# Kernel tuning notes

Measured on AMD Instinct MI355X. Metric: run time of the kernel, lower is better.

Reference implementation:

```python
import jax, jax.numpy as jnp
import numpy as np

N, E, D, H, C, G, L = 50000, 1250000, 128, 64, 10, 128, 2


def setup_inputs() -> dict:
    key = jax.random.key(0)
    ks = jax.random.split(key, 18)
    s = lambda fan_in: 1.0 / np.sqrt(fan_in)
    inp = {
        "x": jax.random.normal(ks[0], (N, D), dtype=jnp.float32),
        "edge_index": jax.random.randint(ks[1], (2, E), 0, N, dtype=jnp.int64),
        "batch": jnp.sort(jax.random.randint(ks[2], (N,), 0, G, dtype=jnp.int64)),
        # node embedding MLP (D->H->H)
        "emb_w1": jax.random.uniform(ks[3], (D, H), jnp.float32, -s(D), s(D)),
        "emb_b1": jnp.zeros((H,), jnp.float32),
        "emb_w2": jax.random.uniform(ks[4], (H, H), jnp.float32, -s(H), s(H)),
        "emb_b2": jnp.zeros((H,), jnp.float32),
        # per-conv-block params, stacked over L layers
        "rel_w": jax.random.uniform(ks[5], (L, H, H), jnp.float32, -s(H), s(H)),
        "rel_b": jnp.zeros((L, H), jnp.float32),
        "root_w": jax.random.uniform(ks[6], (L, H, H), jnp.float32, -s(H), s(H)),
        "post_w1": jax.random.uniform(ks[7], (L, H, H), jnp.float32, -s(H), s(H)),
        "post_b1": jnp.zeros((L, H), jnp.float32),
        "post_w2": jax.random.uniform(ks[8], (L, H, H), jnp.float32, -s(H), s(H)),
        "post_b2": jnp.zeros((L, H), jnp.float32),
        # classifier
        "cls_w": jax.random.uniform(ks[9], (H, C), jnp.float32, -s(H), s(H)),
        "cls_b": jnp.zeros((C,), jnp.float32),
    }
    return inp


def _mlp(h, w1, b1, w2, b2):
    # Linear -> relu -> (dropout: identity in eval) -> Linear
    return jax.nn.relu(h @ w1 + b1) @ w2 + b2


def reference(x, edge_index, batch, emb_w1, emb_b1, emb_w2, emb_b2,
              rel_w, rel_b, root_w, post_w1, post_b1, post_w2, post_b2,
              cls_w, cls_b):
    src, dst = edge_index[0], edge_index[1]
    h = _mlp(x, emb_w1, emb_b1, emb_w2, emb_b2)  # [N,H]
    deg = jax.ops.segment_sum(jnp.ones((E,), h.dtype), dst, num_segments=N)
    inv_deg = 1.0 / jnp.maximum(deg, 1.0)  # mean aggregation, isolated nodes -> 0
    for l in range(L):
        agg = jax.ops.segment_sum(h[src], dst, num_segments=N) * inv_deg[:, None]
        h = agg @ rel_w[l] + rel_b[l] + h @ root_w[l]  # GraphConv (lin_root bias-free)
        h = _mlp(h, post_w1[l], post_b1[l], post_w2[l], post_b2[l])
        h = jax.nn.relu(h)  # dropout is identity in eval
    cnt = jax.ops.segment_sum(jnp.ones((N,), h.dtype), batch, num_segments=G)
    pooled = jax.ops.segment_sum(h, batch, num_segments=G) / jnp.maximum(cnt, 1.0)[:, None]
    return pooled @ cls_w + cls_b  # [G,C]
```

## Files before the change

kernel.cpp:

```cpp
#include <hip/hip_runtime.h>

typedef unsigned int u32;
typedef unsigned short u16;

#define NN 50000
#define EE 1250000
#define DD 128
#define HH 64
#define NCLS 10
#define NG 128
#define MAXDEG 80

#define NTILES ((NN + 63) / 64)
#define LDSW 68

#define PBUK 392
#define SBLK 128
#define CHUNK ((EE + SBLK - 1) / SBLK)
#define NDP  (PBUK * 128)

#define NWMAT 8
#define WT_LO (NWMAT * 4096)


__device__ __forceinline__ u32 f2bf(float f) {
    u32 u = __float_as_uint(f);
    return (u + 0x7FFFu + ((u >> 16) & 1u)) >> 16;
}
__device__ __forceinline__ float bf2f(u16 v) {
    return __uint_as_float(((u32)v) << 16);
}

typedef __attribute__((ext_vector_type(8))) short bf16x8;
typedef __attribute__((ext_vector_type(4))) float f32x4;


__device__ __forceinline__ void load_w(const float* __restrict__ g, float (*wS)[LDSW], int t) {
    #pragma unroll
    for (int r = 0; r < 4; ++r) {
        int idx = r * 256 + t;
        int k = idx >> 4, f4 = idx & 15;
        float4 v = *(const float4*)(g + k * 64 + f4 * 4);
        *(float4*)&wS[k][f4 * 4] = v;
    }
}

__device__ __forceinline__ void load_inT(const float* __restrict__ g, int ld, int c0,
                                         float (*iS)[LDSW], int t, int nb) {
    #pragma unroll
    for (int r = 0; r < 4; ++r) {
        int idx = r * 256 + t;
        int n = idx >> 4, k4 = idx & 15;
        int node = nb + n;
        if (node >= NN) node = NN - 1;
        float4 v = *(const float4*)(g + (size_t)node * ld + c0 + k4 * 4);
        int k0 = k4 * 4;
        int nx = n ^ k0;
        iS[k0 + 0][nx] = v.x;
        iS[k0 + 1][nx] = v.y;
        iS[k0 + 2][nx] = v.z;
        iS[k0 + 3][nx] = v.w;
    }
}

__device__ __forceinline__ void gemm_acc(const float (*iS)[LDSW], const float (*wS)[LDSW],
                                         float acc[4][4], int tx, int ty) {
    #pragma unroll 8
    for (int k = 0; k < 64; ++k) {
        const float4 wv = *(const float4*)&wS[k][tx * 4];
        const float4 iv = *(const float4*)&iS[k][(ty * 4) ^ (k & 60)];
        acc[0][0] += iv.x * wv.x; acc[0][1] += iv.x * wv.y; acc[0][2] += iv.x * wv.z; acc[0][3] += iv.x * wv.w;
        acc[1][0] += iv.y * wv.x; acc[1][1] += iv.y * wv.y; acc[1][2] += iv.y * wv.z; acc[1][3] += iv.y * wv.w;
        acc[2][0] += iv.z * wv.x; acc[2][1] += iv.z * wv.y; acc[2][2] += iv.z * wv.z; acc[2][3] += iv.z * wv.w;
        acc[3][0] += iv.w * wv.x; acc[3][1] += iv.w * wv.y; acc[3][2] += iv.w * wv.z; acc[3][3] += iv.w * wv.w;
    }
}

__device__ __forceinline__ void store_accT(float (*iS)[LDSW], const float acc[4][4], int tx, int ty) {
    #pragma unroll
    for (int i = 0; i < 4; ++i) {
        int k = tx * 4 + i;
        *(float4*)&iS[k][(ty * 4) ^ (tx * 4)] =
            make_float4(acc[0][i], acc[1][i], acc[2][i], acc[3][i]);
    }
}

__device__ __forceinline__ void init_bias(float acc[4][4], const float* __restrict__ b, int tx) {
    float4 bv = *(const float4*)(b + tx * 4);
    #pragma unroll
    for (int j = 0; j < 4; ++j) { acc[j][0] = bv.x; acc[j][1] = bv.y; acc[j][2] = bv.z; acc[j][3] = bv.w; }
}

__device__ __forceinline__ void relu_acc(float acc[4][4]) {
    #pragma unroll
    for (int j = 0; j < 4; ++j)
        #pragma unroll
        for (int i = 0; i < 4; ++i) acc[j][i] = fmaxf(acc[j][i], 0.0f);
}

__device__ __forceinline__ void store_hb(u16* __restrict__ hb, const float acc[4][4],
                                         int tx, int ty, int nb) {
    #pragma unroll
    for (int j = 0; j < 4; ++j) {
        int node = nb + ty * 4 + j;
        if (node < NN) {
            u32 p0 = f2bf(acc[j][0]) | (f2bf(acc[j][1]) << 16);
            u32 p1 = f2bf(acc[j][2]) | (f2bf(acc[j][3]) << 16);
            u32* q = (u32*)(hb + (size_t)node * HH) + tx * 2;
            q[0] = p0; q[1] = p1;
        }
    }
}


__global__ __launch_bounds__(256) void k_embed_psort(
    const float* __restrict__ x,
    const float* __restrict__ w1, const float* __restrict__ b1,
    const float* __restrict__ w2, const float* __restrict__ b2,
    u16* __restrict__ hb,
    const int* __restrict__ ei, u32* __restrict__ bedges,
    int* __restrict__ gboff, int* __restrict__ ghist,
    const float* __restrict__ rel_w, const float* __restrict__ root_w,
    const float* __restrict__ pw1, const float* __restrict__ pw2,
    u16* __restrict__ wtb) {
    __shared__ __align__(16) char smem[2 * 64 * LDSW * 4];
    const int t = threadIdx.x;

    if (blockIdx.x < NTILES) {
        float (*wS)[LDSW] = (float (*)[LDSW])smem;
        float (*iS)[LDSW] = (float (*)[LDSW])(smem + 64 * LDSW * 4);
        const int tx = t & 15, ty = t >> 4;
        const int nb = blockIdx.x * 64;

        float acc[4][4];
        init_bias(acc, b1, tx);
        load_w(w1, wS, t);
        load_inT(x, DD, 0, iS, t, nb);
        __syncthreads();
        gemm_acc(iS, wS, acc, tx, ty);
        __syncthreads();
        load_w(w1 + 64 * 64, wS, t);
        load_inT(x, DD, 64, iS, t, nb);
        __syncthreads();
        gemm_acc(iS, wS, acc, tx, ty);
        __syncthreads();
        relu_acc(acc);
        store_accT(iS, acc, tx, ty);
        load_w(w2, wS, t);
        __syncthreads();
        float acc2[4][4];
        init_bias(acc2, b2, tx);
        gemm_acc(iS, wS, acc2, tx, ty);
        store_hb(hb, acc2, tx, ty, nb);
    } else if (blockIdx.x < NTILES + SBLK) {
        int* hist  = (int*)smem;
        int* boffS = hist + PBUK;
        int* wsum  = boffS + PBUK;
        const int cb = blockIdx.x - NTILES;
        const int base = cb * CHUNK;
        const int n = min(CHUNK, EE - base);

        for (int b = t; b < PBUK; b += 256) hist[b] = 0;
        __syncthreads();
        for (int i = t; i < n; i += 256) {
            int src = ei[base + i];
            int dst = ei[EE + base + i];
            if ((unsigned)src < NN && (unsigned)dst < NN)
                atomicAdd(&hist[dst >> 7], 1);
        }
        __syncthreads();
        int v = 0, h0 = 0;
        if (t < PBUK / 2) { h0 = hist[2 * t]; v = h0 + hist[2 * t + 1]; }
        int lane = t & 63, wd = t >> 6;
        int incl = v;
        #pragma unroll
        for (int d = 1; d < 64; d <<= 1) {
            int tt = __shfl_up(incl, d);
            if (lane >= d) incl += tt;
        }
        if (lane == 63) wsum[wd] = incl;
        __syncthreads();
        int woff = 0;
        for (int w = 0; w < wd; ++w) woff += wsum[w];
        if (t < PBUK / 2) {
            int excl = woff + incl - v;
            boffS[2 * t] = excl;
            boffS[2 * t + 1] = excl + h0;
        }
        __syncthreads();
        for (int b = t; b < PBUK; b += 256) {
            gboff[cb * PBUK + b] = boffS[b];
            ghist[cb * PBUK + b] = hist[b];
        }
        __syncthreads();
        for (int b = t; b < PBUK; b += 256) hist[b] = 0;
        __syncthreads();
        for (int i = t; i < n; i += 256) {
            int src = ei[base + i];
            int dst = ei[EE + base + i];
            if ((unsigned)src < NN && (unsigned)dst < NN) {
                int b = dst >> 7;
                int p = atomicAdd(&hist[b], 1);
                bedges[base + boffS[b] + p] = ((u32)src << 7) | (u32)(dst & 127);
            }
        }
    } else {
        const int m = blockIdx.x - NTILES - SBLK;
        const int layer = m >> 2, which = m & 3;
        const float* srcw =
            (which == 0 ? rel_w : which == 1 ? root_w : which == 2 ? pw1 : pw2)
            + (size_t)layer * HH * HH;
        float* ldsf = (float*)smem;
        #pragma unroll
        for (int r = 0; r < 16; ++r) {
            int idx = r * 256 + t;
            int k = idx >> 6, n = idx & 63;
            ldsf[k * 65 + n] = srcw[k * 64 + n];
        }
        __syncthreads();
        #pragma unroll
        for (int r = 0; r < 16; ++r) {
            int idx = r * 256 + t;
            int n = idx >> 6, k = idx & 63;
            float v = ldsf[k * 65 + n];
            u16 hi = (u16)f2bf(v);
            u16 lo = (u16)f2bf(v - bf2f(hi));
            wtb[m * 4096 + n * 64 + k] = hi;
            wtb[WT_LO + m * 4096 + n * 64 + k] = lo;
        }
    }
}


__global__ __launch_bounds__(256) void k_adj(const u32* __restrict__ bedges,
                                             const int* __restrict__ gboff,
                                             const int* __restrict__ ghist,
                                             u16* __restrict__ slots,
                                             int* __restrict__ deg,
                                             float* __restrict__ pooled) {
    __shared__ u16 ls[128 * MAXDEG];
    __shared__ int lc[128];
    const int b = blockIdx.x, t = threadIdx.x;
    const int lane = t & 63, wid = t >> 6;
    if (b < (NG * HH) / 256) pooled[b * 256 + t] = 0.0f;
    if (t < 128) lc[t] = 0;
    __syncthreads();
    for (int sb = wid; sb < SBLK; sb += 4) {
        int off = gboff[sb * PBUK + b];
        int cnt = ghist[sb * PBUK + b];
        int gbase = sb * CHUNK + off;
        for (int i = lane; i < cnt; i += 64) {
            u32 p = bedges[gbase + i];
            int o = (int)(p & 127u);
            int src = (int)(p >> 7);
            int pos = atomicAdd(&lc[o], 1);
            if (pos < MAXDEG) ls[o * MAXDEG + pos] = (u16)src;
        }
    }
    __syncthreads();
    u32* gs = (u32*)(slots + (size_t)b * 128 * MAXDEG);
    const u32* lsu = (const u32*)ls;
    for (int i = t; i < 128 * MAXDEG / 2; i += 256) gs[i] = lsu[i];
    if (t < 128) deg[b * 128 + t] = lc[t];
}


__global__ __launch_bounds__(256) void k_agg(
    const u16* __restrict__ hb, const int* __restrict__ deg,
    const u16* __restrict__ slots, u16* __restrict__ aggb) {
    const int wid = threadIdx.x >> 6, lane = threadIdx.x & 63;
    const int nA = blockIdx.x * 8 + wid * 2;
    if (nA >= NN) return;
    const int nB = nA + 1;
    const int dA = deg[nA];
    const int dB = (nB < NN) ? deg[nB] : 0;
    const int mA = min(dA, MAXDEG), mB = min(dB, MAXDEG);
    const u16* srA = slots + (size_t)nA * MAXDEG;
    const u16* srB = slots + (size_t)nB * MAXDEG;
    const u32* rowA = (const u32*)srA;
    const u32* rowB = (const u32*)srB;
    float sA = 0.0f, sB = 0.0f;
    const int mm = max(mA, mB);
    for (int e = 0; e + 8 <= mm; e += 8) {
        const int hx = e >> 1;
        const bool pA = (e + 8 <= mA), pB = (e + 8 <= mB);
        float a0=0,a1=0,a2=0,a3=0,a4=0,a5=0,a6=0,a7=0;
        float b0=0,b1=0,b2=0,b3=0,b4=0,b5=0,b6=0,b7=0;
        if (pA) {
            u32 u0 = rowA[hx], u1 = rowA[hx+1], u2 = rowA[hx+2], u3 = rowA[hx+3];
            a0 = bf2f(hb[(size_t)(u0 & 0xffffu) * HH + lane]);
            a1 = bf2f(hb[(size_t)(u0 >> 16) * HH + lane]);
            a2 = bf2f(hb[(size_t)(u1 & 0xffffu) * HH + lane]);
            a3 = bf2f(hb[(size_t)(u1 >> 16) * HH + lane]);
            a4 = bf2f(hb[(size_t)(u2 & 0xffffu) * HH + lane]);
            a5 = bf2f(hb[(size_t)(u2 >> 16) * HH + lane]);
            a6 = bf2f(hb[(size_t)(u3 & 0xffffu) * HH + lane]);
            a7 = bf2f(hb[(size_t)(u3 >> 16) * HH + lane]);
        }
        if (pB) {
            u32 u0 = rowB[hx], u1 = rowB[hx+1], u2 = rowB[hx+2], u3 = rowB[hx+3];
            b0 = bf2f(hb[(size_t)(u0 & 0xffffu) * HH + lane]);
            b1 = bf2f(hb[(size_t)(u0 >> 16) * HH + lane]);
            b2 = bf2f(hb[(size_t)(u1 & 0xffffu) * HH + lane]);
            b3 = bf2f(hb[(size_t)(u1 >> 16) * HH + lane]);
            b4 = bf2f(hb[(size_t)(u2 & 0xffffu) * HH + lane]);
            b5 = bf2f(hb[(size_t)(u2 >> 16) * HH + lane]);
            b6 = bf2f(hb[(size_t)(u3 & 0xffffu) * HH + lane]);
            b7 = bf2f(hb[(size_t)(u3 >> 16) * HH + lane]);
        }
        if (pA) sA += ((a0 + a1) + (a2 + a3)) + ((a4 + a5) + (a6 + a7));
        if (pB) sB += ((b0 + b1) + (b2 + b3)) + ((b4 + b5) + (b6 + b7));
    }
    for (int e = mA & ~7; e < mA; ++e)
        sA += bf2f(hb[(size_t)srA[e] * HH + lane]);
    for (int e = mB & ~7; e < mB; ++e)
        sB += bf2f(hb[(size_t)srB[e] * HH + lane]);
    aggb[(size_t)nA * HH + lane] = (u16)f2bf(sA * (1.0f / (float)max(dA, 1)));
    if (nB < NN)
        aggb[(size_t)nB * HH + lane] = (u16)f2bf(sB * (1.0f / (float)max(dB, 1)));
}


__global__ __launch_bounds__(256) void k_dense(
    u16* __restrict__ hb, const u16* __restrict__ aggb,
    const u16* __restrict__ wt,
    const float* __restrict__ relb,
    const float* __restrict__ pb1, const float* __restrict__ pb2,
    const int* __restrict__ batch, float* __restrict__ pooled, int do_pool) {
    __shared__ __align__(16) u16 acts[2][64][72];
    const int t = threadIdx.x;
    const int w = t >> 6;
    const int l = t & 63;
    const int lr = l & 15, lg = l >> 4;
    const int rowb = w * 16;
    const int nb = blockIdx.x * 64;
    int nodeA = nb + rowb + lr;
    if (nodeA >= NN) nodeA = NN - 1;

    const u16* w_rel = wt;
    const u16* w_root = wt + 4096;
    const u16* w_p1  = wt + 2 * 4096;
    const u16* w_p2  = wt + 3 * 4096;

    const u16* agp = aggb + (size_t)nodeA * HH + lg * 8;
    const u16* hbp = hb   + (size_t)nodeA * HH + lg * 8;
    bf16x8 a0 = *(const bf16x8*)agp;
    bf16x8 a1 = *(const bf16x8*)(agp + 32);
    bf16x8 h0 = *(const bf16x8*)hbp;
    bf16x8 h1 = *(const bf16x8*)(hbp + 32);

    f32x4 acc[4];
    #pragma unroll
    for (int tt = 0; tt < 4; ++tt) {
        float b = relb[tt * 16 + lr];
        acc[tt] = (f32x4){b, b, b, b};
    }
    #pragma unroll
    for (int tt = 0; tt < 4; ++tt) {
        const u16* pr = w_rel  + (tt * 16 + lr) * 64 + lg * 8;
        const u16* po = w_root + (tt * 16 + lr) * 64 + lg * 8;
        acc[tt] = __builtin_amdgcn_mfma_f32_16x16x32_bf16(a0, *(const bf16x8*)pr,                acc[tt], 0, 0, 0);
        acc[tt] = __builtin_amdgcn_mfma_f32_16x16x32_bf16(a1, *(const bf16x8*)(pr + 32),         acc[tt], 0, 0, 0);
        acc[tt] = __builtin_amdgcn_mfma_f32_16x16x32_bf16(a0, *(const bf16x8*)(pr + WT_LO),      acc[tt], 0, 0, 0);
        acc[tt] = __builtin_amdgcn_mfma_f32_16x16x32_bf16(a1, *(const bf16x8*)(pr + WT_LO + 32), acc[tt], 0, 0, 0);
        acc[tt] = __builtin_amdgcn_mfma_f32_16x16x32_bf16(h0, *(const bf16x8*)po,                acc[tt], 0, 0, 0);
        acc[tt] = __builtin_amdgcn_mfma_f32_16x16x32_bf16(h1, *(const bf16x8*)(po + 32),         acc[tt], 0, 0, 0);
        acc[tt] = __builtin_amdgcn_mfma_f32_16x16x32_bf16(h0, *(const bf16x8*)(po + WT_LO),      acc[tt], 0, 0, 0);
        acc[tt] = __builtin_amdgcn_mfma_f32_16x16x32_bf16(h1, *(const bf16x8*)(po + WT_LO + 32), acc[tt], 0, 0, 0);
    }
    #pragma unroll
    for (int tt = 0; tt < 4; ++tt)
        #pragma unroll
        for (int r = 0; r < 4; ++r)
            acts[0][rowb + lg * 4 + r][tt * 16 + lr] = (u16)f2bf(acc[tt][r]);
    __syncthreads();

    bf16x8 c0 = *(const bf16x8*)&acts[0][rowb + lr][lg * 8];
    bf16x8 c1 = *(const bf16x8*)&acts[0][rowb + lr][32 + lg * 8];
    f32x4 acc2[4];
    #pragma unroll
    for (int tt = 0; tt < 4; ++tt) {
        float b = pb1[tt * 16 + lr];
        acc2[tt] = (f32x4){b, b, b, b};
    }
    #pragma unroll
    for (int tt = 0; tt < 4; ++tt) {
        const u16* pr = w_p1 + (tt * 16 + lr) * 64 + lg * 8;
        acc2[tt] = __builtin_amdgcn_mfma_f32_16x16x32_bf16(c0, *(const bf16x8*)pr,                acc2[tt], 0, 0, 0);
        acc2[tt] = __builtin_amdgcn_mfma_f32_16x16x32_bf16(c1, *(const bf16x8*)(pr + 32),         acc2[tt], 0, 0, 0);
        acc2[tt] = __builtin_amdgcn_mfma_f32_16x16x32_bf16(c0, *(const bf16x8*)(pr + WT_LO),      acc2[tt], 0, 0, 0);
        acc2[tt] = __builtin_amdgcn_mfma_f32_16x16x32_bf16(c1, *(const bf16x8*)(pr + WT_LO + 32), acc2[tt], 0, 0, 0);
    }
    #pragma unroll
    for (int tt = 0; tt < 4; ++tt)
        #pragma unroll
        for (int r = 0; r < 4; ++r)
            acts[1][rowb + lg * 4 + r][tt * 16 + lr] = (u16)f2bf(fmaxf(acc2[tt][r], 0.0f));
    __syncthreads();

    bf16x8 d0 = *(const bf16x8*)&acts[1][rowb + lr][lg * 8];
    bf16x8 d1 = *(const bf16x8*)&acts[1][rowb + lr][32 + lg * 8];
    f32x4 acc3[4];
    #pragma unroll
    for (int tt = 0; tt < 4; ++tt) {
        float b = pb2[tt * 16 + lr];
        acc3[tt] = (f32x4){b, b, b, b};
    }
    #pragma unroll
    for (int tt = 0; tt < 4; ++tt) {
        const u16* pr = w_p2 + (tt * 16 + lr) * 64 + lg * 8;
        acc3[tt] = __builtin_amdgcn_mfma_f32_16x16x32_bf16(d0, *(const bf16x8*)pr,                acc3[tt], 0, 0, 0);
        acc3[tt] = __builtin_amdgcn_mfma_f32_16x16x32_bf16(d1, *(const bf16x8*)(pr + 32),         acc3[tt], 0, 0, 0);
        acc3[tt] = __builtin_amdgcn_mfma_f32_16x16x32_bf16(d0, *(const bf16x8*)(pr + WT_LO),      acc3[tt], 0, 0, 0);
        acc3[tt] = __builtin_amdgcn_mfma_f32_16x16x32_bf16(d1, *(const bf16x8*)(pr + WT_LO + 32), acc3[tt], 0, 0, 0);
    }

    if (!do_pool) {
        #pragma unroll
        for (int tt = 0; tt < 4; ++tt)
            #pragma unroll
            for (int r = 0; r < 4; ++r) {
                int node = nb + rowb + lg * 4 + r;
                if (node < NN)
                    hb[(size_t)node * HH + tt * 16 + lr] = (u16)f2bf(fmaxf(acc3[tt][r], 0.0f));
            }
    } else {
        #pragma unroll
        for (int tt = 0; tt < 4; ++tt)
            #pragma unroll
            for (int r = 0; r < 4; ++r)
                acts[0][rowb + lg * 4 + r][tt * 16 + lr] = (u16)f2bf(fmaxf(acc3[tt][r], 0.0f));
        __syncthreads();
        if (t < HH) {
            const int f = t;
            const int n1 = min(64, NN - nb);
            int cur = batch[nb];
            float s = 0.0f;
            for (int i = 0; i < n1; ++i) {
                int g = batch[nb + i];
                if (g != cur) {
                    if ((unsigned)cur < NG) atomicAdd(&pooled[cur * HH + f], s);
                    s = 0.0f; cur = g;
                }
                s += bf2f(acts[0][i][f]);
            }
            if ((unsigned)cur < NG) atomicAdd(&pooled[cur * HH + f], s);
        }
    }
}


__global__ void k_cls(const float* __restrict__ pooled, const int* __restrict__ batch,
                      const float* __restrict__ w, const float* __restrict__ b,
                      float* __restrict__ out) {
    const int g = blockIdx.x;
    const int t = threadIdx.x;
    if (t >= NCLS) return;
    int lo = 0, hi = NN;
    while (lo < hi) { int mid = (lo + hi) >> 1; if (batch[mid] < g) lo = mid + 1; else hi = mid; }
    const int beg = lo;
    lo = 0; hi = NN;
    while (lo < hi) { int mid = (lo + hi) >> 1; if (batch[mid] < g + 1) lo = mid + 1; else hi = mid; }
    const int cnt = lo - beg;
    const float inv = 1.0f / (float)max(cnt, 1);
    float o = b[t];
    #pragma unroll 8
    for (int k = 0; k < HH; ++k) o += pooled[g * HH + k] * inv * w[k * NCLS + t];
    out[g * NCLS + t] = o;
}


extern "C" void kernel_launch(void* const* d_in, const int* in_sizes, int n_in,
                              void* d_out, int out_size, void* d_ws, size_t ws_size,
                              hipStream_t stream) {
    const float* x      = (const float*)d_in[0];
    const int*   ei     = (const int*)d_in[1];
    const int*   batch  = (const int*)d_in[2];
    const float* emb_w1 = (const float*)d_in[3];
    const float* emb_b1 = (const float*)d_in[4];
    const float* emb_w2 = (const float*)d_in[5];
    const float* emb_b2 = (const float*)d_in[6];
    const float* rel_w  = (const float*)d_in[7];
    const float* rel_b  = (const float*)d_in[8];
    const float* root_w = (const float*)d_in[9];
    const float* pw1    = (const float*)d_in[10];
    const float* pb1    = (const float*)d_in[11];
    const float* pw2    = (const float*)d_in[12];
    const float* pb2    = (const float*)d_in[13];
    const float* cls_w  = (const float*)d_in[14];
    const float* cls_b  = (const float*)d_in[15];
    float* out = (float*)d_out;

    char* ws = (char*)d_ws;
    size_t off = 0;
    auto alloc = [&](size_t bytes) -> void* {
        off = (off + 255) & ~(size_t)255;
        void* p = ws + off;
        off += bytes;
        return p;
    };
    u16*   hb     = (u16*)alloc((size_t)NN * HH * 2);
    u16*   aggb   = (u16*)alloc((size_t)NN * HH * 2);
    u32*   bedges = (u32*)aggb;
    u16*   slots  = (u16*)alloc((size_t)NDP * MAXDEG * 2);
    int*   deg    = (int*)alloc((size_t)NDP * 4);
    int*   gboff  = (int*)alloc((size_t)SBLK * PBUK * 4);
    int*   ghist  = (int*)alloc((size_t)SBLK * PBUK * 4);
    float* pooled = (float*)alloc((size_t)NG * HH * 4);
    u16*   wtb    = (u16*)alloc((size_t)2 * NWMAT * 4096 * 2);

    k_embed_psort<<<NTILES + SBLK + NWMAT, 256, 0, stream>>>(
        x, emb_w1, emb_b1, emb_w2, emb_b2, hb, ei, bedges, gboff, ghist,
        rel_w, root_w, pw1, pw2, wtb);
    k_adj<<<PBUK, 256, 0, stream>>>(bedges, gboff, ghist, slots, deg, pooled);
    k_agg<<<(NN + 7) / 8, 256, 0, stream>>>(hb, deg, slots, aggb);
    k_dense<<<NTILES, 256, 0, stream>>>(hb, aggb, wtb, rel_b, pb1, pb2, batch, pooled, 0);
    k_agg<<<(NN + 7) / 8, 256, 0, stream>>>(hb, deg, slots, aggb);
    k_dense<<<NTILES, 256, 0, stream>>>(hb, aggb, wtb + 4 * 4096,
                                        rel_b + HH, pb1 + HH, pb2 + HH,
                                        batch, pooled, 1);
    k_cls<<<NG, 64, 0, stream>>>(pooled, batch, cls_w, cls_b, out);
}
```

Before: 316.0 us.

## Move embedding MLP to split-bf16 MFMA and vectorize aggregation with sentinel padding

The embedding MLP moves from a scalar fp32 LDS GEMM to MFMA bf16 instructions, using hi/lo split precision on both inputs and weights to approximate fp32 accuracy. Weight transposition and splitting moves into a separate small prep kernel that runs first. The aggregation kernel is rewritten so each half-wave handles one node and loads two features per lane with 16-wide unrolled gathers. Slot rows are padded with a sentinel index that points to an extra zero row appended to hb, which removes the tail loops. This adds one kernel launch and padded gathers that read the zero row.

```diff
diff --git a/kernel.cpp b/kernel.cpp
--- a/kernel.cpp
+++ b/kernel.cpp
@@ -12,15 +12,18 @@
 #define MAXDEG 80
 
 #define NTILES ((NN + 63) / 64)
-#define LDSW 68
 
 #define PBUK 392
 #define SBLK 128
 #define CHUNK ((EE + SBLK - 1) / SBLK)
 #define NDP  (PBUK * 128)
 
-#define NWMAT 8
-#define WT_LO (NWMAT * 4096)
+#define WT_LO  (8 * 4096)
+#define WT_E1  (16 * 4096)
+#define WT_E1L (WT_E1 + 8192)
+#define WT_E2  (WT_E1 + 16384)
+#define WT_E2L (WT_E2 + 4096)
+#define WT_TOT (WT_E2 + 8192)
 
 
 __device__ __forceinline__ u32 f2bf(float f) {
@@ -35,79 +38,71 @@
 typedef __attribute__((ext_vector_type(4))) float f32x4;
 
 
-__device__ __forceinline__ void load_w(const float* __restrict__ g, float (*wS)[LDSW], int t) {
-    #pragma unroll
-    for (int r = 0; r < 4; ++r) {
-        int idx = r * 256 + t;
-        int k = idx >> 4, f4 = idx & 15;
-        float4 v = *(const float4*)(g + k * 64 + f4 * 4);
-        *(float4*)&wS[k][f4 * 4] = v;
-    }
-}
-
-__device__ __forceinline__ void load_inT(const float* __restrict__ g, int ld, int c0,
-                                         float (*iS)[LDSW], int t, int nb) {
-    #pragma unroll
-    for (int r = 0; r < 4; ++r) {
-        int idx = r * 256 + t;
-        int n = idx >> 4, k4 = idx & 15;
-        int node = nb + n;
-        if (node >= NN) node = NN - 1;
-        float4 v = *(const float4*)(g + (size_t)node * ld + c0 + k4 * 4);
-        int k0 = k4 * 4;
-        int nx = n ^ k0;
-        iS[k0 + 0][nx] = v.x;
-        iS[k0 + 1][nx] = v.y;
-        iS[k0 + 2][nx] = v.z;
-        iS[k0 + 3][nx] = v.w;
-    }
-}
-
-__device__ __forceinline__ void gemm_acc(const float (*iS)[LDSW], const float (*wS)[LDSW],
-                                         float acc[4][4], int tx, int ty) {
-    #pragma unroll 8
-    for (int k = 0; k < 64; ++k) {
-        const float4 wv = *(const float4*)&wS[k][tx * 4];
-        const float4 iv = *(const float4*)&iS[k][(ty * 4) ^ (k & 60)];
-        acc[0][0] += iv.x * wv.x; acc[0][1] += iv.x * wv.y; acc[0][2] += iv.x * wv.z; acc[0][3] += iv.x * wv.w;
-        acc[1][0] += iv.y * wv.x; acc[1][1] += iv.y * wv.y; acc[1][2] += iv.y * wv.z; acc[1][3] += iv.y * wv.w;
-        acc[2][0] += iv.z * wv.x; acc[2][1] += iv.z * wv.y; acc[2][2] += iv.z * wv.z; acc[2][3] += iv.z * wv.w;
-        acc[3][0] += iv.w * wv.x; acc[3][1] += iv.w * wv.y; acc[3][2] += iv.w * wv.z; acc[3][3] += iv.w * wv.w;
-    }
-}
-
-__device__ __forceinline__ void store_accT(float (*iS)[LDSW], const float acc[4][4], int tx, int ty) {
-    #pragma unroll
-    for (int i = 0; i < 4; ++i) {
-        int k = tx * 4 + i;
-        *(float4*)&iS[k][(ty * 4) ^ (tx * 4)] =
-            make_float4(acc[0][i], acc[1][i], acc[2][i], acc[3][i]);
-    }
-}
-
-__device__ __forceinline__ void init_bias(float acc[4][4], const float* __restrict__ b, int tx) {
-    float4 bv = *(const float4*)(b + tx * 4);
-    #pragma unroll
-    for (int j = 0; j < 4; ++j) { acc[j][0] = bv.x; acc[j][1] = bv.y; acc[j][2] = bv.z; acc[j][3] = bv.w; }
-}
-
-__device__ __forceinline__ void relu_acc(float acc[4][4]) {
-    #pragma unroll
-    for (int j = 0; j < 4; ++j)
-        #pragma unroll
-        for (int i = 0; i < 4; ++i) acc[j][i] = fmaxf(acc[j][i], 0.0f);
-}
-
-__device__ __forceinline__ void store_hb(u16* __restrict__ hb, const float acc[4][4],
-                                         int tx, int ty, int nb) {
-    #pragma unroll
-    for (int j = 0; j < 4; ++j) {
-        int node = nb + ty * 4 + j;
-        if (node < NN) {
-            u32 p0 = f2bf(acc[j][0]) | (f2bf(acc[j][1]) << 16);
-            u32 p1 = f2bf(acc[j][2]) | (f2bf(acc[j][3]) << 16);
-            u32* q = (u32*)(hb + (size_t)node * HH) + tx * 2;
-            q[0] = p0; q[1] = p1;
+__global__ __launch_bounds__(256) void k_wprep(
+    const float* __restrict__ rel_w, const float* __restrict__ root_w,
+    const float* __restrict__ pw1, const float* __restrict__ pw2,
+    const float* __restrict__ ew1, const float* __restrict__ ew2,
+    u16* __restrict__ wtb) {
+    __shared__ float ldsf[128 * 65];
+    const int t = threadIdx.x;
+    const int m = blockIdx.x;
+    if (m < 8) {
+        const int layer = m >> 2, which = m & 3;
+        const float* srcw =
+            (which == 0 ? rel_w : which == 1 ? root_w : which == 2 ? pw1 : pw2)
+            + (size_t)layer * HH * HH;
+        #pragma unroll
+        for (int r = 0; r < 16; ++r) {
+            int idx = r * 256 + t;
+            int k = idx >> 6, n = idx & 63;
+            ldsf[k * 65 + n] = srcw[idx];
+        }
+        __syncthreads();
+        #pragma unroll
+        for (int r = 0; r < 16; ++r) {
+            int idx = r * 256 + t;
+            int n = idx >> 6, k = idx & 63;
+            float v = ldsf[k * 65 + n];
+            u16 hi = (u16)f2bf(v);
+            u16 lo = (u16)f2bf(v - bf2f(hi));
+            wtb[m * 4096 + idx] = hi;
+            wtb[WT_LO + m * 4096 + idx] = lo;
+        }
+    } else if (m == 8) {
+        #pragma unroll
+        for (int r = 0; r < 32; ++r) {
+            int idx = r * 256 + t;
+            int k = idx >> 6, n = idx & 63;
+            ldsf[k * 65 + n] = ew1[idx];
+        }
+        __syncthreads();
+        #pragma unroll
+        for (int r = 0; r < 32; ++r) {
+            int idx = r * 256 + t;
+            int n = idx >> 7, k = idx & 127;
+            float v = ldsf[k * 65 + n];
+            u16 hi = (u16)f2bf(v);
+            u16 lo = (u16)f2bf(v - bf2f(hi));
+            wtb[WT_E1 + idx] = hi;
+            wtb[WT_E1L + idx] = lo;
+        }
+    } else {
+        #pragma unroll
+        for (int r = 0; r < 16; ++r) {
+            int idx = r * 256 + t;
+            int k = idx >> 6, n = idx & 63;
+            ldsf[k * 65 + n] = ew2[idx];
+        }
+        __syncthreads();
+        #pragma unroll
+        for (int r = 0; r < 16; ++r) {
+            int idx = r * 256 + t;
+            int n = idx >> 6, k = idx & 63;
+            float v = ldsf[k * 65 + n];
+            u16 hi = (u16)f2bf(v);
+            u16 lo = (u16)f2bf(v - bf2f(hi));
+            wtb[WT_E2 + idx] = hi;
+            wtb[WT_E2L + idx] = lo;
         }
     }
 }
@@ -115,44 +110,100 @@
 
 __global__ __launch_bounds__(256) void k_embed_psort(
     const float* __restrict__ x,
-    const float* __restrict__ w1, const float* __restrict__ b1,
-    const float* __restrict__ w2, const float* __restrict__ b2,
+    const float* __restrict__ b1, const float* __restrict__ b2,
+    const u16* __restrict__ wtb,
     u16* __restrict__ hb,
     const int* __restrict__ ei, u32* __restrict__ bedges,
-    int* __restrict__ gboff, int* __restrict__ ghist,
-    const float* __restrict__ rel_w, const float* __restrict__ root_w,
-    const float* __restrict__ pw1, const float* __restrict__ pw2,
-    u16* __restrict__ wtb) {
-    __shared__ __align__(16) char smem[2 * 64 * LDSW * 4];
+    int* __restrict__ gboff, int* __restrict__ ghist) {
+    __shared__ __align__(16) char smem[2 * 64 * 72 * 2];
     const int t = threadIdx.x;
 
     if (blockIdx.x < NTILES) {
-        float (*wS)[LDSW] = (float (*)[LDSW])smem;
-        float (*iS)[LDSW] = (float (*)[LDSW])(smem + 64 * LDSW * 4);
-        const int tx = t & 15, ty = t >> 4;
+        u16* acts0 = (u16*)smem;
+        u16* acts1 = (u16*)smem + 64 * 72;
+        const int l = t & 63;
+        const int lr = l & 15, lg = l >> 4;
+        const int rowb = (t >> 6) * 16;
         const int nb = blockIdx.x * 64;
-
-        float acc[4][4];
-        init_bias(acc, b1, tx);
-        load_w(w1, wS, t);
-        load_inT(x, DD, 0, iS, t, nb);
-        __syncthreads();
-        gemm_acc(iS, wS, acc, tx, ty);
-        __syncthreads();
-        load_w(w1 + 64 * 64, wS, t);
-        load_inT(x, DD, 64, iS, t, nb);
-        __syncthreads();
-        gemm_acc(iS, wS, acc, tx, ty);
-        __syncthreads();
-        relu_acc(acc);
-        store_accT(iS, acc, tx, ty);
-        load_w(w2, wS, t);
-        __syncthreads();
-        float acc2[4][4];
-        init_bias(acc2, b2, tx);
-        gemm_acc(iS, wS, acc2, tx, ty);
-        store_hb(hb, acc2, tx, ty, nb);
-    } else if (blockIdx.x < NTILES + SBLK) {
+        int nodeA = nb + rowb + lr;
+        if (nodeA >= NN) nodeA = NN - 1;
+        const float* xp = x + (size_t)nodeA * DD + lg * 8;
+
+        f32x4 acc[4];
+        #pragma unroll
+        for (int tt = 0; tt < 4; ++tt) {
+            float b = b1[tt * 16 + lr];
+            acc[tt] = (f32x4){b, b, b, b};
+        }
+        #pragma unroll
+        for (int kc = 0; kc < 4; ++kc) {
+            float4 v0 = *(const float4*)(xp + kc * 32);
+            float4 v1 = *(const float4*)(xp + kc * 32 + 4);
+            float vv[8] = {v0.x, v0.y, v0.z, v0.w, v1.x, v1.y, v1.z, v1.w};
+            bf16x8 xh, xl;
+            #pragma unroll
+            for (int j = 0; j < 8; ++j) {
+                u16 hi = (u16)f2bf(vv[j]);
+                xh[j] = (short)hi;
+                xl[j] = (short)(u16)f2bf(vv[j] - bf2f(hi));
+            }
+            #pragma unroll
+            for (int tt = 0; tt < 4; ++tt) {
+                const u16* ph = wtb + WT_E1 + (tt * 16 + lr) * 128 + kc * 32 + lg * 8;
+                const u16* pl = wtb + WT_E1L + (tt * 16 + lr) * 128 + kc * 32 + lg * 8;
+                bf16x8 wh = *(const bf16x8*)ph;
+                bf16x8 wl = *(const bf16x8*)pl;
+                acc[tt] = __builtin_amdgcn_mfma_f32_16x16x32_bf16(xh, wh, acc[tt], 0, 0, 0);
+                acc[tt] = __builtin_amdgcn_mfma_f32_16x16x32_bf16(xl, wh, acc[tt], 0, 0, 0);
+                acc[tt] = __builtin_amdgcn_mfma_f32_16x16x32_bf16(xh, wl, acc[tt], 0, 0, 0);
+            }
+        }
+        #pragma unroll
+        for (int tt = 0; tt < 4; ++tt)
+            #pragma unroll
+            for (int r = 0; r < 4; ++r) {
+                float v = fmaxf(acc[tt][r], 0.0f);
+                u16 hi = (u16)f2bf(v);
+                u16 lo = (u16)f2bf(v - bf2f(hi));
+                acts0[(rowb + lg * 4 + r) * 72 + tt * 16 + lr] = hi;
+                acts1[(rowb + lg * 4 + r) * 72 + tt * 16 + lr] = lo;
+            }
+        __syncthreads();
+
+        bf16x8 c0h = *(const bf16x8*)&acts0[(rowb + lr) * 72 + lg * 8];
+        bf16x8 c1h = *(const bf16x8*)&acts0[(rowb + lr) * 72 + 32 + lg * 8];
+        bf16x8 c0l = *(const bf16x8*)&acts1[(rowb + lr) * 72 + lg * 8];
+        bf16x8 c1l = *(const bf16x8*)&acts1[(rowb + lr) * 72 + 32 + lg * 8];
+        f32x4 acc2[4];
+        #pragma unroll
+        for (int tt = 0; tt < 4; ++tt) {
+            float b = b2[tt * 16 + lr];
+            acc2[tt] = (f32x4){b, b, b, b};
+        }
+        #pragma unroll
+        for (int tt = 0; tt < 4; ++tt) {
+            const u16* ph = wtb + WT_E2 + (tt * 16 + lr) * 64 + lg * 8;
+            const u16* pl = wtb + WT_E2L + (tt * 16 + lr) * 64 + lg * 8;
+            bf16x8 wh0 = *(const bf16x8*)ph;
+            bf16x8 wh1 = *(const bf16x8*)(ph + 32);
+            bf16x8 wl0 = *(const bf16x8*)pl;
+            bf16x8 wl1 = *(const bf16x8*)(pl + 32);
+            acc2[tt] = __builtin_amdgcn_mfma_f32_16x16x32_bf16(c0h, wh0, acc2[tt], 0, 0, 0);
+            acc2[tt] = __builtin_amdgcn_mfma_f32_16x16x32_bf16(c1h, wh1, acc2[tt], 0, 0, 0);
+            acc2[tt] = __builtin_amdgcn_mfma_f32_16x16x32_bf16(c0l, wh0, acc2[tt], 0, 0, 0);
+            acc2[tt] = __builtin_amdgcn_mfma_f32_16x16x32_bf16(c1l, wh1, acc2[tt], 0, 0, 0);
+            acc2[tt] = __builtin_amdgcn_mfma_f32_16x16x32_bf16(c0h, wl0, acc2[tt], 0, 0, 0);
+            acc2[tt] = __builtin_amdgcn_mfma_f32_16x16x32_bf16(c1h, wl1, acc2[tt], 0, 0, 0);
+        }
+        #pragma unroll
+        for (int tt = 0; tt < 4; ++tt)
+            #pragma unroll
+            for (int r = 0; r < 4; ++r) {
+                int node = nb + rowb + lg * 4 + r;
+                if (node < NN)
+                    hb[(size_t)node * HH + tt * 16 + lr] = (u16)f2bf(acc2[tt][r]);
+            }
+    } else {
         int* hist  = (int*)smem;
         int* boffS = hist + PBUK;
         int* wsum  = boffS + PBUK;
@@ -204,30 +255,6 @@
                 bedges[base + boffS[b] + p] = ((u32)src << 7) | (u32)(dst & 127);
             }
         }
-    } else {
-        const int m = blockIdx.x - NTILES - SBLK;
-        const int layer = m >> 2, which = m & 3;
-        const float* srcw =
-            (which == 0 ? rel_w : which == 1 ? root_w : which == 2 ? pw1 : pw2)
-            + (size_t)layer * HH * HH;
-        float* ldsf = (float*)smem;
-        #pragma unroll
-        for (int r = 0; r < 16; ++r) {
-            int idx = r * 256 + t;
-            int k = idx >> 6, n = idx & 63;
-            ldsf[k * 65 + n] = srcw[k * 64 + n];
-        }
-        __syncthreads();
-        #pragma unroll
-        for (int r = 0; r < 16; ++r) {
-            int idx = r * 256 + t;
-            int n = idx >> 6, k = idx & 63;
-            float v = ldsf[k * 65 + n];
-            u16 hi = (u16)f2bf(v);
-            u16 lo = (u16)f2bf(v - bf2f(hi));
-            wtb[m * 4096 + n * 64 + k] = hi;
-            wtb[WT_LO + m * 4096 + n * 64 + k] = lo;
-        }
     }
 }
 
@@ -237,13 +264,20 @@
                                              const int* __restrict__ ghist,
                                              u16* __restrict__ slots,
                                              int* __restrict__ deg,
-                                             float* __restrict__ pooled) {
+                                             float* __restrict__ pooled,
+                                             u16* __restrict__ hb) {
     __shared__ u16 ls[128 * MAXDEG];
     __shared__ int lc[128];
     const int b = blockIdx.x, t = threadIdx.x;
     const int lane = t & 63, wid = t >> 6;
     if (b < (NG * HH) / 256) pooled[b * 256 + t] = 0.0f;
+    if (b == 0 && t < 32) ((u32*)hb)[NN * (HH / 2) + t] = 0;
     if (t < 128) lc[t] = 0;
+    {
+        const u32 sent = ((u32)NN << 16) | (u32)NN;
+        u32* lsu = (u32*)ls;
+        for (int i = t; i < 128 * MAXDEG / 2; i += 256) lsu[i] = sent;
+    }
     __syncthreads();
     for (int sb = wid; sb < SBLK; sb += 4) {
         int off = gboff[sb * PBUK + b];
@@ -269,55 +303,58 @@
     const u16* __restrict__ hb, const int* __restrict__ deg,
     const u16* __restrict__ slots, u16* __restrict__ aggb) {
     const int wid = threadIdx.x >> 6, lane = threadIdx.x & 63;
-    const int nA = blockIdx.x * 8 + wid * 2;
-    if (nA >= NN) return;
-    const int nB = nA + 1;
-    const int dA = deg[nA];
-    const int dB = (nB < NN) ? deg[nB] : 0;
-    const int mA = min(dA, MAXDEG), mB = min(dB, MAXDEG);
-    const u16* srA = slots + (size_t)nA * MAXDEG;
-    const u16* srB = slots + (size_t)nB * MAXDEG;
-    const u32* rowA = (const u32*)srA;
-    const u32* rowB = (const u32*)srB;
-    float sA = 0.0f, sB = 0.0f;
-    const int mm = max(mA, mB);
-    for (int e = 0; e + 8 <= mm; e += 8) {
-        const int hx = e >> 1;
-        const bool pA = (e + 8 <= mA), pB = (e + 8 <= mB);
-        float a0=0,a1=0,a2=0,a3=0,a4=0,a5=0,a6=0,a7=0;
-        float b0=0,b1=0,b2=0,b3=0,b4=0,b5=0,b6=0,b7=0;
-        if (pA) {
-            u32 u0 = rowA[hx], u1 = rowA[hx+1], u2 = rowA[hx+2], u3 = rowA[hx+3];
-            a0 = bf2f(hb[(size_t)(u0 & 0xffffu) * HH + lane]);
-            a1 = bf2f(hb[(size_t)(u0 >> 16) * HH + lane]);
-            a2 = bf2f(hb[(size_t)(u1 & 0xffffu) * HH + lane]);
-            a3 = bf2f(hb[(size_t)(u1 >> 16) * HH + lane]);
-            a4 = bf2f(hb[(size_t)(u2 & 0xffffu) * HH + lane]);
-            a5 = bf2f(hb[(size_t)(u2 >> 16) * HH + lane]);
-            a6 = bf2f(hb[(size_t)(u3 & 0xffffu) * HH + lane]);
-            a7 = bf2f(hb[(size_t)(u3 >> 16) * HH + lane]);
-        }
-        if (pB) {
-            u32 u0 = rowB[hx], u1 = rowB[hx+1], u2 = rowB[hx+2], u3 = rowB[hx+3];
-            b0 = bf2f(hb[(size_t)(u0 & 0xffffu) * HH + lane]);
-            b1 = bf2f(hb[(size_t)(u0 >> 16) * HH + lane]);
-            b2 = bf2f(hb[(size_t)(u1 & 0xffffu) * HH + lane]);
-            b3 = bf2f(hb[(size_t)(u1 >> 16) * HH + lane]);
-            b4 = bf2f(hb[(size_t)(u2 & 0xffffu) * HH + lane]);
-            b5 = bf2f(hb[(size_t)(u2 >> 16) * HH + lane]);
-            b6 = bf2f(hb[(size_t)(u3 & 0xffffu) * HH + lane]);
-            b7 = bf2f(hb[(size_t)(u3 >> 16) * HH + lane]);
-        }
-        if (pA) sA += ((a0 + a1) + (a2 + a3)) + ((a4 + a5) + (a6 + a7));
-        if (pB) sB += ((b0 + b1) + (b2 + b3)) + ((b4 + b5) + (b6 + b7));
-    }
-    for (int e = mA & ~7; e < mA; ++e)
-        sA += bf2f(hb[(size_t)srA[e] * HH + lane]);
-    for (int e = mB & ~7; e < mB; ++e)
-        sB += bf2f(hb[(size_t)srB[e] * HH + lane]);
-    aggb[(size_t)nA * HH + lane] = (u16)f2bf(sA * (1.0f / (float)max(dA, 1)));
-    if (nB < NN)
-        aggb[(size_t)nB * HH + lane] = (u16)f2bf(sB * (1.0f / (float)max(dB, 1)));
+    const int half = lane >> 5, fl = lane & 31;
+    const int n0 = blockIdx.x * 8 + wid * 2;
+    if (n0 >= NN) return;
+    const int n = n0 + half;
+    const bool valid = n < NN;
+    const int d = valid ? deg[n] : 0;
+    const int m = min(d, MAXDEG);
+    const int mp = (m + 15) & ~15;
+    const u32* row = (const u32*)(slots + (size_t)n * MAXDEG);
+    float s0 = 0.0f, s1 = 0.0f;
+    for (int e = 0; e < mp; e += 16) {
+        const u32* rp = row + (e >> 1);
+        uint4 i0 = *(const uint4*)rp;
+        uint4 i1 = *(const uint4*)(rp + 4);
+        u32 v0 = *(const u32*)(hb + (size_t)(i0.x & 0xffffu) * HH + 2 * fl);
+        u32 v1 = *(const u32*)(hb + (size_t)(i0.x >> 16)    * HH + 2 * fl);
+        u32 v2 = *(const u32*)(hb + (size_t)(i0.y & 0xffffu) * HH + 2 * fl);
+        u32 v3 = *(const u32*)(hb + (size_t)(i0.y >> 16)    * HH + 2 * fl);
+        u32 v4 = *(const u32*)(hb + (size_t)(i0.z & 0xffffu) * HH + 2 * fl);
+        u32 v5 = *(const u32*)(hb + (size_t)(i0.z >> 16)    * HH + 2 * fl);
+        u32 v6 = *(const u32*)(hb + (size_t)(i0.w & 0xffffu) * HH + 2 * fl);
+        u32 v7 = *(const u32*)(hb + (size_t)(i0.w >> 16)    * HH + 2 * fl);
+        u32 v8 = *(const u32*)(hb + (size_t)(i1.x & 0xffffu) * HH + 2 * fl);
+        u32 v9 = *(const u32*)(hb + (size_t)(i1.x >> 16)    * HH + 2 * fl);
+        u32 va = *(const u32*)(hb + (size_t)(i1.y & 0xffffu) * HH + 2 * fl);
+        u32 vb = *(const u32*)(hb + (size_t)(i1.y >> 16)    * HH + 2 * fl);
+        u32 vc = *(const u32*)(hb + (size_t)(i1.z & 0xffffu) * HH + 2 * fl);
+        u32 vd = *(const u32*)(hb + (size_t)(i1.z >> 16)    * HH + 2 * fl);
+        u32 ve = *(const u32*)(hb + (size_t)(i1.w & 0xffffu) * HH + 2 * fl);
+        u32 vf = *(const u32*)(hb + (size_t)(i1.w >> 16)    * HH + 2 * fl);
+        s0 += ((bf2f((u16)(v0 & 0xffffu)) + bf2f((u16)(v1 & 0xffffu)))
+             + (bf2f((u16)(v2 & 0xffffu)) + bf2f((u16)(v3 & 0xffffu))))
+            + ((bf2f((u16)(v4 & 0xffffu)) + bf2f((u16)(v5 & 0xffffu)))
+             + (bf2f((u16)(v6 & 0xffffu)) + bf2f((u16)(v7 & 0xffffu))));
+        s0 += ((bf2f((u16)(v8 & 0xffffu)) + bf2f((u16)(v9 & 0xffffu)))
+             + (bf2f((u16)(va & 0xffffu)) + bf2f((u16)(vb & 0xffffu))))
+            + ((bf2f((u16)(vc & 0xffffu)) + bf2f((u16)(vd & 0xffffu)))
+             + (bf2f((u16)(ve & 0xffffu)) + bf2f((u16)(vf & 0xffffu))));
+        s1 += ((bf2f((u16)(v0 >> 16)) + bf2f((u16)(v1 >> 16)))
+             + (bf2f((u16)(v2 >> 16)) + bf2f((u16)(v3 >> 16))))
+            + ((bf2f((u16)(v4 >> 16)) + bf2f((u16)(v5 >> 16)))
+             + (bf2f((u16)(v6 >> 16)) + bf2f((u16)(v7 >> 16))));
+        s1 += ((bf2f((u16)(v8 >> 16)) + bf2f((u16)(v9 >> 16)))
+             + (bf2f((u16)(va >> 16)) + bf2f((u16)(vb >> 16))))
+            + ((bf2f((u16)(vc >> 16)) + bf2f((u16)(vd >> 16)))
+             + (bf2f((u16)(ve >> 16)) + bf2f((u16)(vf >> 16))));
+    }
+    if (valid) {
+        float inv = 1.0f / (float)max(d, 1);
+        u32 p = f2bf(s0 * inv) | (f2bf(s1 * inv) << 16);
+        ((u32*)aggb)[(size_t)n * (HH / 2) + fl] = p;
+    }
 }
 
 
@@ -499,7 +536,7 @@
         off += bytes;
         return p;
     };
-    u16*   hb     = (u16*)alloc((size_t)NN * HH * 2);
+    u16*   hb     = (u16*)alloc((size_t)(NN + 1) * HH * 2);
     u16*   aggb   = (u16*)alloc((size_t)NN * HH * 2);
     u32*   bedges = (u32*)aggb;
     u16*   slots  = (u16*)alloc((size_t)NDP * MAXDEG * 2);
@@ -507,12 +544,12 @@
     int*   gboff  = (int*)alloc((size_t)SBLK * PBUK * 4);
     int*   ghist  = (int*)alloc((size_t)SBLK * PBUK * 4);
     float* pooled = (float*)alloc((size_t)NG * HH * 4);
-    u16*   wtb    = (u16*)alloc((size_t)2 * NWMAT * 4096 * 2);
-
-    k_embed_psort<<<NTILES + SBLK + NWMAT, 256, 0, stream>>>(
-        x, emb_w1, emb_b1, emb_w2, emb_b2, hb, ei, bedges, gboff, ghist,
-        rel_w, root_w, pw1, pw2, wtb);
-    k_adj<<<PBUK, 256, 0, stream>>>(bedges, gboff, ghist, slots, deg, pooled);
+    u16*   wtb    = (u16*)alloc((size_t)WT_TOT * 2);
+
+    k_wprep<<<10, 256, 0, stream>>>(rel_w, root_w, pw1, pw2, emb_w1, emb_w2, wtb);
+    k_embed_psort<<<NTILES + SBLK, 256, 0, stream>>>(
+        x, emb_b1, emb_b2, wtb, hb, ei, bedges, gboff, ghist);
+    k_adj<<<PBUK, 256, 0, stream>>>(bedges, gboff, ghist, slots, deg, pooled, hb);
     k_agg<<<(NN + 7) / 8, 256, 0, stream>>>(hb, deg, slots, aggb);
     k_dense<<<NTILES, 256, 0, stream>>>(hb, aggb, wtb, rel_b, pb1, pb2, batch, pooled, 0);
     k_agg<<<(NN + 7) / 8, 256, 0, stream>>>(hb, deg, slots, aggb);
```

Result: faster. 285.9 us (-9.5%).
